# Performance work log

Hardware: AMD Instinct MI355X
Metric: run time of the kernel (lower is better)

The kernel has to match this reference:

```python
import jax, jax.numpy as jnp
import numpy as np

NU, NI, F, H, D = 100000, 50000, 256, 8, 64
E1, E2 = 300000, 300000
SLOPE = 0.2  # DGL GATConv default negative_slope


def setup_inputs() -> dict:
    key = jax.random.key(0)
    ks = jax.random.split(key, 20)
    p = lambda k, sh: jax.random.normal(k, sh, jnp.float32) * 0.1
    return {
        "h_user": jax.random.normal(ks[0], (NU, F), jnp.float32),
        "h_item": jax.random.normal(ks[1], (NI, F), jnp.float32),
        "src_u2i": jax.random.randint(ks[2], (E1,), 0, NU),
        "dst_u2i": jax.random.randint(ks[3], (E1,), 0, NI),
        "src_i2u": jax.random.randint(ks[4], (E2,), 0, NI),
        "dst_i2u": jax.random.randint(ks[5], (E2,), 0, NU),
        "W_src_u2i": p(ks[6], (F, H * D)), "W_dst_u2i": p(ks[7], (F, H * D)),
        "al_u2i": p(ks[8], (H, D)), "ar_u2i": p(ks[9], (H, D)),
        "bias_u2i": jnp.zeros((H * D,), jnp.float32), "W_res_u2i": p(ks[10], (F, H * D)),
        "W_src_i2u": p(ks[11], (F, H * D)), "W_dst_i2u": p(ks[12], (F, H * D)),
        "al_i2u": p(ks[13], (H, D)), "ar_i2u": p(ks[14], (H, D)),
        "bias_i2u": jnp.zeros((H * D,), jnp.float32), "W_res_i2u": p(ks[15], (F, H * D)),
    }


def _gat(h_src, h_dst, src, dst, Ws, Wd, al, ar, b, Wr, n_dst):
    # linear projections -> [N, H, D]
    fs = (h_src @ Ws).reshape(-1, H, D)
    fd = (h_dst @ Wd).reshape(-1, H, D)
    el = jnp.einsum('nhd,hd->nh', fs, al)   # a_l . Wh_src
    er = jnp.einsum('nhd,hd->nh', fd, ar)   # a_r . Wh_dst
    e = jax.nn.leaky_relu(el[src] + er[dst], SLOPE)  # [E, H]
    # segment softmax over incoming edges of each dst node
    m = jax.ops.segment_max(e, dst, num_segments=n_dst)
    m = jnp.where(jnp.isfinite(m), m, jnp.float32(0))  # nodes with no edges
    ex = jnp.exp(e - m[dst])
    s = jax.ops.segment_sum(ex, dst, num_segments=n_dst)
    a = ex / s[dst]                                   # [E, H]
    # weighted scatter-sum of gathered source features
    out = jax.ops.segment_sum(a[:, :, None] * fs[src], dst, num_segments=n_dst)
    res = (h_dst @ Wr).reshape(-1, H, D)              # residual projection
    return out + res + b.reshape(1, H, D)


def reference(h_user, h_item, src_u2i, dst_u2i, src_i2u, dst_i2u,
              W_src_u2i, W_dst_u2i, al_u2i, ar_u2i, bias_u2i, W_res_u2i,
              W_src_i2u, W_dst_i2u, al_i2u, ar_i2u, bias_i2u, W_res_i2u):
    out_item = _gat(h_user, h_item, src_u2i, dst_u2i,
                    W_src_u2i, W_dst_u2i, al_u2i, ar_u2i, bias_u2i, W_res_u2i, NI)
    out_user = _gat(h_item, h_user, src_i2u, dst_i2u,
                    W_src_i2u, W_dst_i2u, al_i2u, ar_i2u, bias_i2u, W_res_i2u, NU)
    return (out_user, out_item)
```

## Files before the change

kernel.cpp:

```cpp
#include <hip/hip_runtime.h>
#include <cstdint>
#include <cstddef>

#define NU_ 100000
#define NI_ 50000
#define F_ 256
#define H_ 8
#define HD_ 512
#define NE_ 300000
#define SLOPE_ 0.2f

#define MPAD_U 100096
#define MPAD_I 50048
#define MT_U (MPAD_U / 128)
#define MT_I (MPAD_I / 128)
#define GEMM_NB ((MT_U + MT_I) * 4)

#define SCAN_N (NI_ + NU_)
#define SCAN_CHUNK 2048
#define SCAN_NB ((SCAN_N + SCAN_CHUNK - 1) / SCAN_CHUNK)

#define PREP_COPY_U (NU_ * F_ / 2048)
#define PREP_COPY_I (NI_ * F_ / 2048)
#define PREP_COPY (PREP_COPY_U + PREP_COPY_I)
#define PREP_WCONV 2048
#define PREP_FOLD 32
#define PREP_HIST ((2 * NE_ + 255) / 256)
#define PREP_NB (PREP_COPY + PREP_WCONV + PREP_FOLD + PREP_HIST)

typedef float f32x4 __attribute__((ext_vector_type(4)));
typedef __bf16 bf16x8 __attribute__((ext_vector_type(8)));
typedef unsigned short u16x8 __attribute__((ext_vector_type(8)));
typedef unsigned short u16x4 __attribute__((ext_vector_type(4)));

static __device__ __forceinline__ unsigned short f2bf_bits(float f) {
  unsigned u = __float_as_uint(f);
  u += 0x7fffu + ((u >> 16) & 1u);
  return (unsigned short)(u >> 16);
}
static __device__ __forceinline__ float bf2f(unsigned short b) {
  return __uint_as_float(((unsigned)b) << 16);
}

#define GLL16(g, l)                                                        \
  __builtin_amdgcn_global_load_lds(                                        \
      (const __attribute__((address_space(1))) void*)(g),                  \
      (__attribute__((address_space(3))) void*)(l), 16, 0, 0)

__global__ __launch_bounds__(256) void prep_kernel(const float* __restrict__ h_user,
                                                   const float* __restrict__ h_item,
                                                   const float* __restrict__ W0,
                                                   const float* __restrict__ W1,
                                                   const float* __restrict__ W2,
                                                   const float* __restrict__ W3,
                                                   const float* __restrict__ Wd0,
                                                   const float* __restrict__ Wd1,
                                                   const float* __restrict__ a0,
                                                   const float* __restrict__ a1,
                                                   const float* __restrict__ a2,
                                                   const float* __restrict__ a3,
                                                   const int* __restrict__ dst_u2i,
                                                   const int* __restrict__ dst_i2u,
                                                   unsigned short* __restrict__ hb_user,
                                                   unsigned short* __restrict__ hb_item,
                                                   unsigned short* __restrict__ Wt,
                                                   unsigned short* __restrict__ wfb,
                                                   int* __restrict__ deg) {
  int bid = blockIdx.x;
  if (bid < PREP_COPY) {
    bool user = bid < PREP_COPY_U;
    const float* h = user ? h_user : h_item;
    unsigned short* hb = user ? hb_user : hb_item;
    size_t base = (size_t)(user ? bid : bid - PREP_COPY_U) * 2048 + threadIdx.x * 8;
    f32x4 a = *(const f32x4*)&h[base];
    f32x4 b = *(const f32x4*)&h[base + 4];
    u16x8 o;
    o[0] = f2bf_bits(a.x); o[1] = f2bf_bits(a.y); o[2] = f2bf_bits(a.z); o[3] = f2bf_bits(a.w);
    o[4] = f2bf_bits(b.x); o[5] = f2bf_bits(b.y); o[6] = f2bf_bits(b.z); o[7] = f2bf_bits(b.w);
    *(u16x8*)&hb[base] = o;
  } else if (bid < PREP_COPY + PREP_WCONV) {
    int idx = (bid - PREP_COPY) * 256 + threadIdx.x;
    int m = idx >> 17;
    int r = idx & 131071;
    const float* W = (m == 0) ? W0 : (m == 1) ? W1 : (m == 2) ? W2 : W3;
    int f = r & 255, c = r >> 8;
    Wt[idx] = f2bf_bits(W[(size_t)f * HD_ + c]);
  } else if (bid < PREP_COPY + PREP_WCONV + PREP_FOLD) {
    int b = bid - PREP_COPY - PREP_WCONV;
    int m = b >> 3;
    int idx = (b & 7) * 256 + threadIdx.x;
    const float* W = (m == 0) ? W0 : (m == 1) ? Wd0 : (m == 2) ? W2 : Wd1;
    const float* av = (m == 0) ? a0 : (m == 1) ? a1 : (m == 2) ? a2 : a3;
    int f = idx & 255, hh = idx >> 8;
    float acc = 0.f;
#pragma unroll 8
    for (int d = 0; d < 64; ++d) acc += W[(size_t)f * HD_ + hh * 64 + d] * av[hh * 64 + d];
    int buf = (m == 0 || m == 3) ? 0 : 1;
    int rowoff = (m == 1 || m == 3) ? 8 : 0;
    wfb[buf * 4096 + (rowoff + hh) * 256 + f] = f2bf_bits(acc);
  } else {
    int e = (bid - PREP_COPY - PREP_WCONV - PREP_FOLD) * 256 + threadIdx.x;
    if (e < NE_) atomicAdd(&deg[dst_u2i[e]], 1);
    else if (e < 2 * NE_) atomicAdd(&deg[NI_ + dst_i2u[e - NE_]], 1);
  }
}

__global__ __launch_bounds__(256) void gemm2_kernel(const unsigned short* __restrict__ hb_user,
                                                    const unsigned short* __restrict__ hb_item,
                                                    const unsigned short* __restrict__ Wt,
                                                    const unsigned short* __restrict__ wfb,
                                                    unsigned short* __restrict__ fs_u2i,
                                                    unsigned short* __restrict__ fs_i2u,
                                                    unsigned short* __restrict__ res_user,
                                                    unsigned short* __restrict__ res_item,
                                                    const float* __restrict__ bias_u2i,
                                                    const float* __restrict__ bias_i2u,
                                                    float* __restrict__ el_u2i,
                                                    float* __restrict__ er_i2u,
                                                    float* __restrict__ el_i2u,
                                                    float* __restrict__ er_u2i,
                                                    const int* __restrict__ deg,
                                                    int* __restrict__ bsum) {
  __shared__ unsigned short lds[2][3][128][32];
  __shared__ unsigned short wflds[2][16][32];
  if (blockIdx.x >= GEMM_NB) {
    int* ilds = (int*)&lds[0][0][0][0];
    int tid = threadIdx.x;
    int base = (blockIdx.x - GEMM_NB) * SCAN_CHUNK + tid * 8;
    int sum = 0;
#pragma unroll
    for (int j = 0; j < 8; ++j) sum += (base + j < SCAN_N) ? deg[base + j] : 0;
    ilds[tid] = sum;
    __syncthreads();
    for (int o = 128; o > 0; o >>= 1) {
      if (tid < o) ilds[tid] += ilds[tid + o];
      __syncthreads();
    }
    if (tid == 0) bsum[blockIdx.x - GEMM_NB] = ilds[0];
    return;
  }
  int bid = blockIdx.x;
  bool user = bid < MT_U * 4;
  if (!user) bid -= MT_U * 4;
  const unsigned short* Ab  = user ? hb_user : hb_item;
  const unsigned short* B1t = user ? (Wt + 0 * HD_ * F_) : (Wt + 2 * HD_ * F_);
  const unsigned short* B2t = user ? (Wt + 3 * HD_ * F_) : (Wt + 1 * HD_ * F_);
  const unsigned short* wfs = user ? wfb : (wfb + 4096);
  unsigned short* fs  = user ? fs_u2i : fs_i2u;
  unsigned short* res = user ? res_user : res_item;
  const float* bias = user ? bias_i2u : bias_u2i;
  int M = user ? NU_ : NI_;

  int tid = threadIdx.x;
  int lane = tid & 63;
  int wave = tid >> 6;
  int wm = wave >> 1, wn = wave & 1;
  int mt = bid >> 2, nt = bid & 3;
  int bm = mt * 128, bn = nt * 128;
  f32x4 acc1[4][4] = {};
  f32x4 acc2[4][4] = {};
  f32x4 acc3[4] = {};
  int lr = lane & 15;
  int kk = (lane >> 4) * 8;

  int r0 = tid >> 2;
  int c0 = (tid & 3) << 3;
  const unsigned short* gA  = &Ab [(size_t)(bm + r0) * 256 + c0];
  const unsigned short* gB1 = &B1t[(size_t)(bn + r0) * 256 + c0];
  const unsigned short* gB2 = &B2t[(size_t)(bn + r0) * 256 + c0];
  const unsigned short* gW  = &wfs[(size_t)(tid >> 2) * 256 + c0];

#define STAGE(buf, t)                                                       \
  do {                                                                      \
    int k0_ = (t) * 32;                                                     \
    GLL16(gA  + k0_,          &lds[buf][0][r0][c0]);                        \
    GLL16(gA  + k0_ + 64*256, &lds[buf][0][r0 + 64][c0]);                   \
    GLL16(gB1 + k0_,          &lds[buf][1][r0][c0]);                        \
    GLL16(gB1 + k0_ + 64*256, &lds[buf][1][r0 + 64][c0]);                   \
    GLL16(gB2 + k0_,          &lds[buf][2][r0][c0]);                        \
    GLL16(gB2 + k0_ + 64*256, &lds[buf][2][r0 + 64][c0]);                   \
    if (nt == 0 && tid < 64) GLL16(gW + k0_, &wflds[buf][tid >> 2][c0]);    \
  } while (0)

  STAGE(0, 0);
  __syncthreads();
  int cur = 0;
#pragma unroll
  for (int t = 0; t < 8; ++t) {
    if (t < 7) STAGE(cur ^ 1, t + 1);
    bf16x8 af[4], b1[4], b2[4];
#pragma unroll
    for (int m = 0; m < 4; ++m)
      af[m] = __builtin_bit_cast(bf16x8, *(const u16x8*)&lds[cur][0][wm * 64 + m * 16 + lr][kk]);
#pragma unroll
    for (int n = 0; n < 4; ++n) {
      b1[n] = __builtin_bit_cast(bf16x8, *(const u16x8*)&lds[cur][1][wn * 64 + n * 16 + lr][kk]);
      b2[n] = __builtin_bit_cast(bf16x8, *(const u16x8*)&lds[cur][2][wn * 64 + n * 16 + lr][kk]);
    }
#pragma unroll
    for (int m = 0; m < 4; ++m)
#pragma unroll
      for (int n = 0; n < 4; ++n) {
        acc1[m][n] = __builtin_amdgcn_mfma_f32_16x16x32_bf16(af[m], b1[n], acc1[m][n], 0, 0, 0);
        acc2[m][n] = __builtin_amdgcn_mfma_f32_16x16x32_bf16(af[m], b2[n], acc2[m][n], 0, 0, 0);
      }
    if (nt == 0) {
      bf16x8 b3 = __builtin_bit_cast(bf16x8, *(const u16x8*)&wflds[cur][lr][kk]);
#pragma unroll
      for (int m = 0; m < 4; ++m)
        acc3[m] = __builtin_amdgcn_mfma_f32_16x16x32_bf16(af[m], b3, acc3[m], 0, 0, 0);
    }
    __syncthreads();
    cur ^= 1;
  }
#undef STAGE

  int rg = (lane >> 4) * 4;
#pragma unroll
  for (int m = 0; m < 4; ++m) {
#pragma unroll
    for (int r = 0; r < 4; ++r) {
      int row = bm + wm * 64 + m * 16 + rg + r;
      if (row >= M) continue;
#pragma unroll
      for (int n = 0; n < 4; ++n) {
        int col = bn + wn * 64 + n * 16 + lr;
        fs[(size_t)row * HD_ + col]  = f2bf_bits(acc1[m][n][r]);
        res[(size_t)row * HD_ + col] = f2bf_bits(acc2[m][n][r] + bias[col]);
      }
    }
  }
  if (nt == 0 && wn == 0) {
    float* elp = user ? el_u2i : el_i2u;
    float* erp = user ? er_i2u : er_u2i;
#pragma unroll
    for (int m = 0; m < 4; ++m) {
#pragma unroll
      for (int r = 0; r < 4; ++r) {
        int row = bm + wm * 64 + m * 16 + rg + r;
        if (row >= M) continue;
        if (lr < 8) elp[(size_t)row * 8 + lr] = acc3[m][r];
        else        erp[(size_t)row * 8 + lr - 8] = acc3[m][r];
      }
    }
  }
}

__global__ __launch_bounds__(256) void scan_apply_kernel(const int* __restrict__ deg,
                                                         const int* __restrict__ bsum,
                                                         int* __restrict__ rowstart,
                                                         int* __restrict__ cursor) {
  __shared__ int sb[128];
  __shared__ int lds[256];
  int tid = threadIdx.x;
  if (tid < 128) sb[tid] = (tid < SCAN_NB) ? bsum[tid] : 0;
  __syncthreads();
  for (int o = 1; o < 128; o <<= 1) {
    int t = (tid < 128 && tid >= o) ? sb[tid - o] : 0;
    __syncthreads();
    if (tid < 128) sb[tid] += t;
    __syncthreads();
  }
  int blockpref = (blockIdx.x == 0) ? 0 : sb[blockIdx.x - 1];
  int base = blockIdx.x * SCAN_CHUNK + tid * 8;
  int v[8];
  int sum = 0;
#pragma unroll
  for (int j = 0; j < 8; ++j) {
    v[j] = (base + j < SCAN_N) ? deg[base + j] : 0;
    sum += v[j];
  }
  lds[tid] = sum;
  __syncthreads();
  for (int o = 1; o < 256; o <<= 1) {
    int t = (tid >= o) ? lds[tid - o] : 0;
    __syncthreads();
    lds[tid] += t;
    __syncthreads();
  }
  int run = blockpref + lds[tid] - sum;
#pragma unroll
  for (int j = 0; j < 8; ++j) {
    if (base + j < SCAN_N) { rowstart[base + j] = run; cursor[base + j] = run; }
    run += v[j];
  }
  if (blockIdx.x == 0 && tid == 0) rowstart[SCAN_N] = 2 * NE_;
}

__global__ __launch_bounds__(256) void bin_kernel(const int* __restrict__ src_u2i,
                                                  const int* __restrict__ dst_u2i,
                                                  const int* __restrict__ src_i2u,
                                                  const int* __restrict__ dst_i2u,
                                                  int* __restrict__ cursor,
                                                  int* __restrict__ ssrc) {
  int e = blockIdx.x * 256 + threadIdx.x;
  int de, se;
  if (e < NE_) { de = dst_u2i[e]; se = src_u2i[e]; }
  else if (e < 2 * NE_) { de = NI_ + dst_i2u[e - NE_]; se = src_i2u[e - NE_]; }
  else return;
  int pos = atomicAdd(&cursor[de], 1);
  ssrc[pos] = se;
}

__global__ __launch_bounds__(256) void accum_kernel(const int* __restrict__ rowstart,
                                                    const int* __restrict__ ssrc,
                                                    const float* __restrict__ el_u2i,
                                                    const float* __restrict__ el_i2u,
                                                    const float* __restrict__ er_u2i,
                                                    const float* __restrict__ er_i2u,
                                                    const unsigned short* __restrict__ fs_u2i,
                                                    const unsigned short* __restrict__ fs_i2u,
                                                    const unsigned short* __restrict__ res_user,
                                                    const unsigned short* __restrict__ res_item,
                                                    float* __restrict__ out_item,
                                                    float* __restrict__ out_user) {
  int n = blockIdx.x * 4 + (threadIdx.x >> 6);
  int lane = threadIdx.x & 63;
  bool item = n < NI_;
  int ln = item ? n : n - NI_;
  const unsigned short* res = item ? res_item : res_user;
  float* out = (item ? out_item : out_user) + (size_t)ln * HD_;
  int r0 = rowstart[n], r1 = rowstart[n + 1];
  float acc[8] = {};
  if (r0 < r1) {
    const float* el = item ? el_u2i : el_i2u;
    const float* er = item ? er_u2i : er_i2u;
    const unsigned short* fs = item ? fs_u2i : fs_i2u;
    int hh = lane >> 3;
    float erh = er[(size_t)ln * 8 + hh];
    float m = -3.0e38f, s = 0.f;
    int k = r0;
    for (; k + 2 <= r1; k += 2) {
      int s0 = ssrc[k], s1 = ssrc[k + 1];
      float e0 = el[(size_t)s0 * 8 + hh] + erh;
      float e1 = el[(size_t)s1 * 8 + hh] + erh;
      e0 = e0 > 0.f ? e0 : SLOPE_ * e0;
      e1 = e1 > 0.f ? e1 : SLOPE_ * e1;
      u16x8 v0 = *(const u16x8*)&fs[(size_t)s0 * HD_ + lane * 8];
      u16x8 v1 = *(const u16x8*)&fs[(size_t)s1 * HD_ + lane * 8];
      float mm = fmaxf(e0, e1);
      if (mm > m) {
        float r = __expf(m - mm);
        s *= r;
#pragma unroll
        for (int j = 0; j < 8; ++j) acc[j] *= r;
        m = mm;
      }
      float x0 = __expf(e0 - m), x1 = __expf(e1 - m);
      s += x0 + x1;
#pragma unroll
      for (int j = 0; j < 8; ++j)
        acc[j] += x0 * bf2f((unsigned short)v0[j]) + x1 * bf2f((unsigned short)v1[j]);
    }
    if (k < r1) {
      int s0 = ssrc[k];
      float e0 = el[(size_t)s0 * 8 + hh] + erh;
      e0 = e0 > 0.f ? e0 : SLOPE_ * e0;
      u16x8 v0 = *(const u16x8*)&fs[(size_t)s0 * HD_ + lane * 8];
      if (e0 > m) {
        float r = __expf(m - e0);
        s *= r;
#pragma unroll
        for (int j = 0; j < 8; ++j) acc[j] *= r;
        m = e0;
      }
      float x0 = __expf(e0 - m);
      s += x0;
#pragma unroll
      for (int j = 0; j < 8; ++j) acc[j] += x0 * bf2f((unsigned short)v0[j]);
    }
    float inv = 1.f / s;
#pragma unroll
    for (int j = 0; j < 8; ++j) acc[j] *= inv;
  }
  u16x8 rv = *(const u16x8*)&res[(size_t)ln * HD_ + lane * 8];
  f32x4 o0, o1;
#pragma unroll
  for (int j = 0; j < 4; ++j) {
    o0[j] = acc[j] + bf2f((unsigned short)rv[j]);
    o1[j] = acc[4 + j] + bf2f((unsigned short)rv[4 + j]);
  }
  float* op = out + lane * 8;
  *(f32x4*)op = o0;
  *(f32x4*)(op + 4) = o1;
}

extern "C" void kernel_launch(void* const* d_in, const int* in_sizes, int n_in,
                              void* d_out, int out_size, void* d_ws, size_t ws_size,
                              hipStream_t stream) {
  const float* h_user    = (const float*)d_in[0];
  const float* h_item    = (const float*)d_in[1];
  const int*   src_u2i   = (const int*)d_in[2];
  const int*   dst_u2i   = (const int*)d_in[3];
  const int*   src_i2u   = (const int*)d_in[4];
  const int*   dst_i2u   = (const int*)d_in[5];
  const float* W_src_u2i = (const float*)d_in[6];
  const float* W_dst_u2i = (const float*)d_in[7];
  const float* al_u2i    = (const float*)d_in[8];
  const float* ar_u2i    = (const float*)d_in[9];
  const float* bias_u2i  = (const float*)d_in[10];
  const float* W_res_u2i = (const float*)d_in[11];
  const float* W_src_i2u = (const float*)d_in[12];
  const float* W_dst_i2u = (const float*)d_in[13];
  const float* al_i2u    = (const float*)d_in[14];
  const float* ar_i2u    = (const float*)d_in[15];
  const float* bias_i2u  = (const float*)d_in[16];
  const float* W_res_i2u = (const float*)d_in[17];

  float* out_user = (float*)d_out;
  float* out_item = (float*)d_out + (size_t)NU_ * HD_;

  char* ws = (char*)d_ws;
  size_t off = 0;
  auto take = [&](size_t bytes) -> char* {
    char* p = ws + off;
    off += (bytes + 255) & ~(size_t)255;
    return p;
  };
  unsigned short* fs_u2i   = (unsigned short*)take((size_t)NU_ * HD_ * 2);
  unsigned short* fs_i2u   = (unsigned short*)take((size_t)NI_ * HD_ * 2);
  unsigned short* res_user = (unsigned short*)take((size_t)NU_ * HD_ * 2);
  unsigned short* res_item = (unsigned short*)take((size_t)NI_ * HD_ * 2);
  unsigned short* hb_user  = (unsigned short*)take((size_t)MPAD_U * F_ * 2);
  unsigned short* hb_item  = (unsigned short*)take((size_t)MPAD_I * F_ * 2);
  unsigned short* Wt  = (unsigned short*)take((size_t)4 * HD_ * F_ * 2);
  unsigned short* wfb = (unsigned short*)take((size_t)2 * 16 * F_ * 2);
  float* el_u2i = (float*)take((size_t)NU_ * 8 * 4);
  float* er_i2u = (float*)take((size_t)NU_ * 8 * 4);
  float* el_i2u = (float*)take((size_t)NI_ * 8 * 4);
  float* er_u2i = (float*)take((size_t)NI_ * 8 * 4);
  int* deg_all      = (int*)take((size_t)SCAN_N * 4);
  int* rowstart_all = (int*)take((size_t)(SCAN_N + 1) * 4);
  int* cursor_all   = (int*)take((size_t)SCAN_N * 4);
  int* bsum         = (int*)take((size_t)128 * 4);
  int* ssrc         = (int*)take((size_t)2 * NE_ * 4);

  hipMemsetAsync(deg_all, 0, (size_t)SCAN_N * 4, stream);

  prep_kernel<<<PREP_NB, 256, 0, stream>>>(h_user, h_item,
                                           W_src_u2i, W_res_u2i, W_src_i2u, W_res_i2u,
                                           W_dst_u2i, W_dst_i2u,
                                           al_u2i, ar_u2i, al_i2u, ar_i2u,
                                           dst_u2i, dst_i2u,
                                           hb_user, hb_item, Wt, wfb, deg_all);

  gemm2_kernel<<<GEMM_NB + SCAN_NB, 256, 0, stream>>>(hb_user, hb_item, Wt, wfb,
                                                      fs_u2i, fs_i2u, res_user, res_item,
                                                      bias_u2i, bias_i2u,
                                                      el_u2i, er_i2u, el_i2u, er_u2i,
                                                      deg_all, bsum);

  scan_apply_kernel<<<SCAN_NB, 256, 0, stream>>>(deg_all, bsum, rowstart_all, cursor_all);
  constexpr int EB2 = (2 * NE_ + 255) / 256;
  bin_kernel<<<EB2, 256, 0, stream>>>(src_u2i, dst_u2i, src_i2u, dst_i2u, cursor_all, ssrc);

  accum_kernel<<<SCAN_N / 4, 256, 0, stream>>>(rowstart_all, ssrc,
                                               el_u2i, el_i2u, er_u2i, er_i2u,
                                               fs_u2i, fs_i2u, res_user, res_item,
                                               out_item, out_user);
}
```

Measured before the change: 508.1 us.

## Swizzle GEMM LDS layout, remap blocks per XCD, and use explicit vmcnt waits

The fused projection GEMM gets three changes. Block indices are remapped so consecutive tiles land on the same XCD for better L2 reuse. Global-to-LDS loads use an XOR column swizzle, with matching swizzled reads, to cut LDS bank conflicts. The syncthreads-based double buffer is replaced with explicit s_waitcnt vmcnt counts plus raw barriers, so the next stage's loads stay in flight during compute. This relies on the per-thread load count matching vmcnt(6), and the nt==0 extra load makes that count uneven across threads, which risks a race if miscounted.

Result: no change. 502.0 us (-1.2%).

```diff
diff --git a/kernel.cpp b/kernel.cpp
--- a/kernel.cpp
+++ b/kernel.cpp
@@ -139,7 +139,12 @@
     if (tid == 0) bsum[blockIdx.x - GEMM_NB] = ilds[0];
     return;
   }
-  int bid = blockIdx.x;
+  int bid;
+  {
+    constexpr int qq = GEMM_NB / 8, rr = GEMM_NB % 8;
+    int xcd = blockIdx.x & 7, sidx = blockIdx.x >> 3;
+    bid = (xcd < rr ? xcd * (qq + 1) : rr * (qq + 1) + (xcd - rr) * qq) + sidx;
+  }
   bool user = bid < MT_U * 4;
   if (!user) bid -= MT_U * 4;
   const unsigned short* Ab  = user ? hb_user : hb_item;
@@ -161,14 +166,15 @@
   f32x4 acc2[4][4] = {};
   f32x4 acc3[4] = {};
   int lr = lane & 15;
-  int kk = (lane >> 4) * 8;
+  int ksw = ((lane >> 4) ^ ((lr >> 1) & 3)) << 3;
 
   int r0 = tid >> 2;
   int c0 = (tid & 3) << 3;
-  const unsigned short* gA  = &Ab [(size_t)(bm + r0) * 256 + c0];
-  const unsigned short* gB1 = &B1t[(size_t)(bn + r0) * 256 + c0];
-  const unsigned short* gB2 = &B2t[(size_t)(bn + r0) * 256 + c0];
-  const unsigned short* gW  = &wfs[(size_t)(tid >> 2) * 256 + c0];
+  int cs = (((tid & 3) ^ ((r0 >> 1) & 3)) << 3);
+  const unsigned short* gA  = &Ab [(size_t)(bm + r0) * 256 + cs];
+  const unsigned short* gB1 = &B1t[(size_t)(bn + r0) * 256 + cs];
+  const unsigned short* gB2 = &B2t[(size_t)(bn + r0) * 256 + cs];
+  const unsigned short* gW  = &wfs[(size_t)(tid >> 2) * 256 + cs];
 
 #define STAGE(buf, t)                                                       \
   do {                                                                      \
@@ -183,19 +189,22 @@
   } while (0)
 
   STAGE(0, 0);
-  __syncthreads();
-  int cur = 0;
 #pragma unroll
   for (int t = 0; t < 8; ++t) {
-    if (t < 7) STAGE(cur ^ 1, t + 1);
+    if (t < 7) STAGE((t + 1) & 1, t + 1);
+    if (t < 7) asm volatile("s_waitcnt vmcnt(6)" ::: "memory");
+    else       asm volatile("s_waitcnt vmcnt(0)" ::: "memory");
+    __builtin_amdgcn_s_barrier();
+    __builtin_amdgcn_sched_barrier(0);
+    const int cb = t & 1;
     bf16x8 af[4], b1[4], b2[4];
 #pragma unroll
     for (int m = 0; m < 4; ++m)
-      af[m] = __builtin_bit_cast(bf16x8, *(const u16x8*)&lds[cur][0][wm * 64 + m * 16 + lr][kk]);
+      af[m] = __builtin_bit_cast(bf16x8, *(const u16x8*)&lds[cb][0][wm * 64 + m * 16 + lr][ksw]);
 #pragma unroll
     for (int n = 0; n < 4; ++n) {
-      b1[n] = __builtin_bit_cast(bf16x8, *(const u16x8*)&lds[cur][1][wn * 64 + n * 16 + lr][kk]);
-      b2[n] = __builtin_bit_cast(bf16x8, *(const u16x8*)&lds[cur][2][wn * 64 + n * 16 + lr][kk]);
+      b1[n] = __builtin_bit_cast(bf16x8, *(const u16x8*)&lds[cb][1][wn * 64 + n * 16 + lr][ksw]);
+      b2[n] = __builtin_bit_cast(bf16x8, *(const u16x8*)&lds[cb][2][wn * 64 + n * 16 + lr][ksw]);
     }
 #pragma unroll
     for (int m = 0; m < 4; ++m)
@@ -205,13 +214,13 @@
         acc2[m][n] = __builtin_amdgcn_mfma_f32_16x16x32_bf16(af[m], b2[n], acc2[m][n], 0, 0, 0);
       }
     if (nt == 0) {
-      bf16x8 b3 = __builtin_bit_cast(bf16x8, *(const u16x8*)&wflds[cur][lr][kk]);
+      bf16x8 b3 = __builtin_bit_cast(bf16x8, *(const u16x8*)&wflds[cb][lr][ksw]);
 #pragma unroll
       for (int m = 0; m < 4; ++m)
         acc3[m] = __builtin_amdgcn_mfma_f32_16x16x32_bf16(af[m], b3, acc3[m], 0, 0, 0);
     }
-    __syncthreads();
-    cur ^= 1;
+    __builtin_amdgcn_sched_barrier(0);
+    __builtin_amdgcn_s_barrier();
   }
 #undef STAGE
 
```
